# Kernel tuning notes

Measured on AMD Instinct MI355X. Metric: run time of the kernel, lower is better.

Reference implementation:

```python
import jax, jax.numpy as jnp
import numpy as np

B, C, S = 32768, 30, 7
COORD, NOOBJ = 5.0, 0.5


def setup_inputs() -> dict:
    key = jax.random.key(0)
    k1, k2, k3 = jax.random.split(key, 3)
    # uniform in [0.05, 1): size loss takes sqrt of raw channels, so keep them positive
    pre = jax.random.uniform(k1, (B, C, S, S), jnp.float32, 0.05, 1.0)
    lab = jax.random.uniform(k2, (B, C, S, S), jnp.float32, 0.05, 1.0)
    # channel 4 of the label is a binary objectness indicator (code tests == 1)
    objm = (jax.random.uniform(k3, (B, S, S)) < 0.3).astype(jnp.float32)
    lab = lab.at[:, 4].set(objm)
    return {"pre": pre, "lab": lab}


def _iou(b1, b2):
    # b1, b2: [B, 4, S, S] with channels (x1, y1, x2, y2); original '+1' pixel convention
    ix1 = jnp.maximum(b1[:, 0], b2[:, 0])
    iy1 = jnp.maximum(b1[:, 1], b2[:, 1])
    ix2 = jnp.minimum(b1[:, 2], b2[:, 2])
    iy2 = jnp.minimum(b1[:, 3], b2[:, 3])
    inter = jnp.maximum(ix2 - ix1 + 1.0, 0.0) * jnp.maximum(iy2 - iy1 + 1.0, 0.0)
    a1 = (b1[:, 2] - b1[:, 0] + 1.0) * (b1[:, 3] - b1[:, 1] + 1.0)
    a2 = (b2[:, 2] - b2[:, 0] + 1.0) * (b2[:, 3] - b2[:, 1] + 1.0)
    return inter / (a1 + a2 - inter)


def reference(pre, lab):
    obj = lab[:, 4] == 1.0                      # [B,S,S] objectness mask
    iou1 = _iou(pre[:, 0:4], lab[:, 0:4])       # box 1 IoU
    iou2 = _iou(pre[:, 5:9], lab[:, 5:9])       # box 2 IoU
    resp1 = iou1 >= iou2                        # box 1 responsible

    # coordinate loss: the px*64 / py*64 grid offsets cancel in (cxl - cxp)
    addr1 = COORD * ((lab[:, 0] - pre[:, 0]) ** 2 + (lab[:, 1] - pre[:, 1]) ** 2)
    addr2 = COORD * ((lab[:, 5] - pre[:, 5]) ** 2 + (lab[:, 6] - pre[:, 6]) ** 2)

    size1 = COORD * ((jnp.sqrt(pre[:, 2]) - jnp.sqrt(lab[:, 2])) ** 2
                     + (jnp.sqrt(pre[:, 3]) - jnp.sqrt(lab[:, 3])) ** 2)
    size2 = COORD * ((jnp.sqrt(pre[:, 7]) - jnp.sqrt(lab[:, 7])) ** 2
                     + (jnp.sqrt(pre[:, 8]) - jnp.sqrt(lab[:, 8])) ** 2)

    # original always uses pre[9] as the responsible confidence (faithful to source)
    conf = NOOBJ * (pre[:, 9] - jnp.where(resp1, iou1, iou2)) ** 2

    obj_terms = jnp.where(resp1, addr1 + size1, addr2 + size2) + conf
    noobj_terms = NOOBJ * (pre[:, 4] + pre[:, 9]) ** 2

    # class loss is accumulated for every cell regardless of objectness
    cls = jnp.sum((pre[:, 10:] - lab[:, 10:]) ** 2)

    total = jnp.sum(jnp.where(obj, obj_terms, noobj_terms)) + cls
    return total / B
```

## Files before the change

kernel.cpp:

```cpp
#include <hip/hip_runtime.h>


#define BATCH 32768
#define S2    49
#define CST   1470
#define NCELL (BATCH * S2)

__device__ __forceinline__ float iou4(float px1, float py1, float px2, float py2,
                                      float lx1, float ly1, float lx2, float ly2) {
    float ix1 = fmaxf(px1, lx1), iy1 = fmaxf(py1, ly1);
    float ix2 = fminf(px2, lx2), iy2 = fminf(py2, ly2);
    float iw = fmaxf(ix2 - ix1 + 1.0f, 0.0f);
    float ih = fmaxf(iy2 - iy1 + 1.0f, 0.0f);
    float inter = iw * ih;
    float a1 = (px2 - px1 + 1.0f) * (py2 - py1 + 1.0f);
    float a2 = (lx2 - lx1 + 1.0f) * (ly2 - ly1 + 1.0f);
    return inter / (a1 + a2 - inter);
}

__global__ __launch_bounds__(256) void yolo_loss_main(const float* __restrict__ pre,
                                                      const float* __restrict__ lab,
                                                      float* __restrict__ partials) {
    float acc = 0.0f;
    const int stride = gridDim.x * blockDim.x;
    for (int cell = blockIdx.x * blockDim.x + threadIdx.x; cell < NCELL; cell += stride) {
        int b = cell / S2;
        int s = cell - b * S2;
        const float* __restrict__ P = pre + b * CST + s;
        const float* __restrict__ L = lab + b * CST + s;

        float p0 = P[0],      p1 = P[S2],     p2 = P[2 * S2], p3 = P[3 * S2], p4 = P[4 * S2];
        float p5 = P[5 * S2], p6 = P[6 * S2], p7 = P[7 * S2], p8 = P[8 * S2], p9 = P[9 * S2];
        float l0 = L[0],      l1 = L[S2],     l2 = L[2 * S2], l3 = L[3 * S2], l4 = L[4 * S2];
        float l5 = L[5 * S2], l6 = L[6 * S2], l7 = L[7 * S2], l8 = L[8 * S2];

        float iou1 = iou4(p0, p1, p2, p3, l0, l1, l2, l3);
        float iou2 = iou4(p5, p6, p7, p8, l5, l6, l7, l8);
        bool resp1 = iou1 >= iou2;

        float d0 = l0 - p0, d1 = l1 - p1, d5 = l5 - p5, d6 = l6 - p6;
        float addr1 = 5.0f * (d0 * d0 + d1 * d1);
        float addr2 = 5.0f * (d5 * d5 + d6 * d6);

        float e2 = sqrtf(p2) - sqrtf(l2), e3 = sqrtf(p3) - sqrtf(l3);
        float e7 = sqrtf(p7) - sqrtf(l7), e8 = sqrtf(p8) - sqrtf(l8);
        float size1 = 5.0f * (e2 * e2 + e3 * e3);
        float size2 = 5.0f * (e7 * e7 + e8 * e8);

        float du = p9 - (resp1 ? iou1 : iou2);
        float conf = 0.5f * du * du;

        float obj_terms = (resp1 ? (addr1 + size1) : (addr2 + size2)) + conf;
        float pn = p4 + p9;
        float noobj = 0.5f * pn * pn;
        float cellv = (l4 == 1.0f) ? obj_terms : noobj;

        float cls = 0.0f;
        #pragma unroll
        for (int c = 10; c < 30; ++c) {
            float d = P[c * S2] - L[c * S2];
            cls += d * d;
        }
        acc += cellv + cls;
    }

    #pragma unroll
    for (int off = 32; off > 0; off >>= 1) acc += __shfl_down(acc, off);

    __shared__ float red[4];
    int lane = threadIdx.x & 63, wid = threadIdx.x >> 6;
    if (lane == 0) red[wid] = acc;
    __syncthreads();
    if (threadIdx.x == 0) partials[blockIdx.x] = red[0] + red[1] + red[2] + red[3];
}

__global__ __launch_bounds__(256) void yolo_loss_final(const float* __restrict__ partials,
                                                       int n, float* __restrict__ out) {
    double v = 0.0;
    for (int i = (int)threadIdx.x; i < n; i += 256) v += (double)partials[i];
    __shared__ double sm[256];
    sm[threadIdx.x] = v;
    __syncthreads();
    for (int s = 128; s > 0; s >>= 1) {
        if ((int)threadIdx.x < s) sm[threadIdx.x] += sm[threadIdx.x + s];
        __syncthreads();
    }
    if (threadIdx.x == 0) out[0] = (float)(sm[0] * (1.0 / (double)BATCH));
}

extern "C" void kernel_launch(void* const* d_in, const int* in_sizes, int n_in,
                              void* d_out, int out_size, void* d_ws, size_t ws_size,
                              hipStream_t stream) {
    const float* pre = (const float*)d_in[0];
    const float* lab = (const float*)d_in[1];
    float* out = (float*)d_out;
    float* partials = (float*)d_ws;

    int nblk = 2048;
    if (ws_size < (size_t)nblk * sizeof(float)) {
        nblk = (int)(ws_size / sizeof(float));
        if (nblk < 1) nblk = 1;
    }

    yolo_loss_main<<<nblk, 256, 0, stream>>>(pre, lab, partials);
    yolo_loss_final<<<1, 256, 0, stream>>>(partials, nblk, out);
}
```

Measured before the change: 82.87 us.

## Stage batch pairs in shared memory with float4 loads before per-cell compute

Each block copies two whole batches of pre and lab into LDS using vectorized float4 loads, then 98 threads compute per-cell losses from shared memory. The goal is wider, fully contiguous global loads in place of strided per-channel scalar loads. The trade-offs are two block barriers per group, most threads idle during compute, no overlap between loading and computing, and higher LDS use. The grid size also changes from 2048 to 1536 blocks.

```diff
diff --git a/kernel.cpp b/kernel.cpp
--- a/kernel.cpp
+++ b/kernel.cpp
@@ -1,10 +1,15 @@
 #include <hip/hip_runtime.h>
 
 
-#define BATCH 32768
-#define S2    49
-#define CST   1470
-#define NCELL (BATCH * S2)
+#define BATCH   32768
+#define S2      49
+#define CPB     1470
+#define NB      2
+#define GFLOATS (NB * CPB)
+#define GVEC    (GFLOATS / 4)
+#define NGROUPS (BATCH / NB)
+#define CELLS   (NB * S2)
+#define NBLK    1536
 
 __device__ __forceinline__ float iou4(float px1, float py1, float px2, float py2,
                                       float lx1, float ly1, float lx2, float ly2) {
@@ -18,60 +23,78 @@
     return inter / (a1 + a2 - inter);
 }
 
-__global__ __launch_bounds__(256) void yolo_loss_main(const float* __restrict__ pre,
-                                                      const float* __restrict__ lab,
+__global__ __launch_bounds__(256) void yolo_loss_main(const float4* __restrict__ pre4,
+                                                      const float4* __restrict__ lab4,
                                                       float* __restrict__ partials) {
+    __shared__ float4 smem[2 * GVEC];
+    __shared__ float red[4];
+    float* preS = (float*)smem;
+    float* labS = (float*)(smem + GVEC);
+    const int tid = threadIdx.x;
+
     float acc = 0.0f;
-    const int stride = gridDim.x * blockDim.x;
-    for (int cell = blockIdx.x * blockDim.x + threadIdx.x; cell < NCELL; cell += stride) {
-        int b = cell / S2;
-        int s = cell - b * S2;
-        const float* __restrict__ P = pre + b * CST + s;
-        const float* __restrict__ L = lab + b * CST + s;
+    for (int g = blockIdx.x; g < NGROUPS; g += gridDim.x) {
+        const float4* __restrict__ ps = pre4 + (size_t)g * GVEC;
+        const float4* __restrict__ ls = lab4 + (size_t)g * GVEC;
+        #pragma unroll
+        for (int k = 0; k < 3; ++k) {
+            int i = tid + k * 256;
+            if (i < GVEC) {
+                smem[i]        = ps[i];
+                smem[GVEC + i] = ls[i];
+            }
+        }
+        __syncthreads();
 
-        float p0 = P[0],      p1 = P[S2],     p2 = P[2 * S2], p3 = P[3 * S2], p4 = P[4 * S2];
-        float p5 = P[5 * S2], p6 = P[6 * S2], p7 = P[7 * S2], p8 = P[8 * S2], p9 = P[9 * S2];
-        float l0 = L[0],      l1 = L[S2],     l2 = L[2 * S2], l3 = L[3 * S2], l4 = L[4 * S2];
-        float l5 = L[5 * S2], l6 = L[6 * S2], l7 = L[7 * S2], l8 = L[8 * S2];
+        if (tid < CELLS) {
+            int bl = tid / S2;
+            int s  = tid - bl * S2;
+            const float* __restrict__ P = preS + bl * CPB + s;
+            const float* __restrict__ L = labS + bl * CPB + s;
 
-        float iou1 = iou4(p0, p1, p2, p3, l0, l1, l2, l3);
-        float iou2 = iou4(p5, p6, p7, p8, l5, l6, l7, l8);
-        bool resp1 = iou1 >= iou2;
+            float p0 = P[0],      p1 = P[S2],     p2 = P[2 * S2], p3 = P[3 * S2], p4 = P[4 * S2];
+            float p5 = P[5 * S2], p6 = P[6 * S2], p7 = P[7 * S2], p8 = P[8 * S2], p9 = P[9 * S2];
+            float l0 = L[0],      l1 = L[S2],     l2 = L[2 * S2], l3 = L[3 * S2], l4 = L[4 * S2];
+            float l5 = L[5 * S2], l6 = L[6 * S2], l7 = L[7 * S2], l8 = L[8 * S2];
 
-        float d0 = l0 - p0, d1 = l1 - p1, d5 = l5 - p5, d6 = l6 - p6;
-        float addr1 = 5.0f * (d0 * d0 + d1 * d1);
-        float addr2 = 5.0f * (d5 * d5 + d6 * d6);
+            float iou1 = iou4(p0, p1, p2, p3, l0, l1, l2, l3);
+            float iou2 = iou4(p5, p6, p7, p8, l5, l6, l7, l8);
+            bool resp1 = iou1 >= iou2;
 
-        float e2 = sqrtf(p2) - sqrtf(l2), e3 = sqrtf(p3) - sqrtf(l3);
-        float e7 = sqrtf(p7) - sqrtf(l7), e8 = sqrtf(p8) - sqrtf(l8);
-        float size1 = 5.0f * (e2 * e2 + e3 * e3);
-        float size2 = 5.0f * (e7 * e7 + e8 * e8);
+            float d0 = l0 - p0, d1 = l1 - p1, d5 = l5 - p5, d6 = l6 - p6;
+            float addr1 = 5.0f * (d0 * d0 + d1 * d1);
+            float addr2 = 5.0f * (d5 * d5 + d6 * d6);
 
-        float du = p9 - (resp1 ? iou1 : iou2);
-        float conf = 0.5f * du * du;
+            float e2 = sqrtf(p2) - sqrtf(l2), e3 = sqrtf(p3) - sqrtf(l3);
+            float e7 = sqrtf(p7) - sqrtf(l7), e8 = sqrtf(p8) - sqrtf(l8);
+            float size1 = 5.0f * (e2 * e2 + e3 * e3);
+            float size2 = 5.0f * (e7 * e7 + e8 * e8);
 
-        float obj_terms = (resp1 ? (addr1 + size1) : (addr2 + size2)) + conf;
-        float pn = p4 + p9;
-        float noobj = 0.5f * pn * pn;
-        float cellv = (l4 == 1.0f) ? obj_terms : noobj;
+            float du = p9 - (resp1 ? iou1 : iou2);
+            float conf = 0.5f * du * du;
 
-        float cls = 0.0f;
-        #pragma unroll
-        for (int c = 10; c < 30; ++c) {
-            float d = P[c * S2] - L[c * S2];
-            cls += d * d;
+            float obj_terms = (resp1 ? (addr1 + size1) : (addr2 + size2)) + conf;
+            float pn = p4 + p9;
+            float noobj = 0.5f * pn * pn;
+            float cellv = (l4 == 1.0f) ? obj_terms : noobj;
+
+            float cls = 0.0f;
+            #pragma unroll
+            for (int c = 10; c < 30; ++c) {
+                float d = P[c * S2] - L[c * S2];
+                cls += d * d;
+            }
+            acc += cellv + cls;
         }
-        acc += cellv + cls;
+        __syncthreads();
     }
 
     #pragma unroll
     for (int off = 32; off > 0; off >>= 1) acc += __shfl_down(acc, off);
-
-    __shared__ float red[4];
-    int lane = threadIdx.x & 63, wid = threadIdx.x >> 6;
+    int lane = tid & 63, wid = tid >> 6;
     if (lane == 0) red[wid] = acc;
     __syncthreads();
-    if (threadIdx.x == 0) partials[blockIdx.x] = red[0] + red[1] + red[2] + red[3];
+    if (tid == 0) partials[blockIdx.x] = red[0] + red[1] + red[2] + red[3];
 }
 
 __global__ __launch_bounds__(256) void yolo_loss_final(const float* __restrict__ partials,
@@ -91,17 +114,17 @@
 extern "C" void kernel_launch(void* const* d_in, const int* in_sizes, int n_in,
                               void* d_out, int out_size, void* d_ws, size_t ws_size,
                               hipStream_t stream) {
-    const float* pre = (const float*)d_in[0];
-    const float* lab = (const float*)d_in[1];
+    const float4* pre4 = (const float4*)d_in[0];
+    const float4* lab4 = (const float4*)d_in[1];
     float* out = (float*)d_out;
     float* partials = (float*)d_ws;
 
-    int nblk = 2048;
+    int nblk = NBLK;
     if (ws_size < (size_t)nblk * sizeof(float)) {
         nblk = (int)(ws_size / sizeof(float));
         if (nblk < 1) nblk = 1;
     }
 
-    yolo_loss_main<<<nblk, 256, 0, stream>>>(pre, lab, partials);
+    yolo_loss_main<<<nblk, 256, 0, stream>>>(pre4, lab4, partials);
     yolo_loss_final<<<1, 256, 0, stream>>>(partials, nblk, out);
 }
```

Measured after the change: 73.01 us. 1.14x faster.
